# Performance work log

Measured on AMD Instinct MI355X. Metric: run time of the kernel, lower is better.

The kernel has to match this reference:

```python
import jax, jax.numpy as jnp
import numpy as np

THRESH = 8000.0  # saturating partial-sum accumulator threshold (thresh=8000 in source)
GROUP = 128      # channel chunk size used by split_tensor_* helpers
EPS = 1e-5

def binarize(x):
    # sign() forward with straight-through estimator (standard BinarizeConv2d behavior)
    return x + jax.lax.stop_gradient(jnp.sign(x) - x)

def psum_conv3x3(x, w):
    """3x3 'same' conv computed as 9 shifted-window partial sums per 128-channel
    group, with the running accumulator saturated to [-THRESH, THRESH] after each
    partial sum (emulating a low-bit hardware accumulator).
    x: [B, C, H, W]; w: [O, C, 3, 3] -> out [B, O, H, W]."""
    B, C, H, W = x.shape
    O = w.shape[0]
    xp = jnp.pad(x, ((0, 0), (0, 0), (1, 1), (1, 1)))
    acc = jnp.zeros((B, O, H, W), dtype=x.dtype)
    n_groups = C // GROUP
    for g in range(n_groups):
        xg = xp[:, g * GROUP:(g + 1) * GROUP]
        wg = w[:, g * GROUP:(g + 1) * GROUP]
        # split_tensor ordering: x1..x9 vary row (dim2) fastest, then col (dim3)
        for col in range(3):
            for row in range(3):
                part = jnp.einsum('bchw,oc->bohw',
                                  xg[:, :, row:row + H, col:col + W],
                                  wg[:, :, row, col])
                acc = jnp.clip(acc + part, -THRESH, THRESH)
    return acc

def batchnorm(x, gamma, beta, mean, var):
    inv = gamma / jnp.sqrt(var + EPS)
    return x * inv[None, :, None, None] + (beta - mean * inv)[None, :, None, None]

def setup_inputs() -> dict:
    key = jax.random.key(0)
    ks = jax.random.split(key, 12)
    B, C, H, W = 64, 128, 56, 56
    return {
        'x': jax.random.normal(ks[0], (B, C, H, W), jnp.float32),
        'w1': jax.random.normal(ks[1], (C, C, 3, 3), jnp.float32),
        'w2': jax.random.normal(ks[2], (C, C, 3, 3), jnp.float32),
        'gamma1': jax.random.uniform(ks[3], (C,), jnp.float32, 0.5, 1.5),
        'beta1': jax.random.normal(ks[4], (C,), jnp.float32) * 0.1,
        'mean1': jax.random.normal(ks[5], (C,), jnp.float32),
        'var1': jax.random.uniform(ks[6], (C,), jnp.float32, 0.5, 1.5),
        'gamma2': jax.random.uniform(ks[7], (C,), jnp.float32, 0.5, 1.5),
        'beta2': jax.random.normal(ks[8], (C,), jnp.float32) * 0.1,
        'mean2': jax.random.normal(ks[9], (C,), jnp.float32),
        'var2': jax.random.uniform(ks[10], (C,), jnp.float32, 0.5, 1.5),
    }

def reference(x, w1, w2, gamma1, beta1, mean1, var1, gamma2, beta2, mean2, var2):
    residual = x
    out = psum_conv3x3(binarize(x), binarize(w1))
    out = batchnorm(out, gamma1, beta1, mean1, var1)
    out = jnp.clip(out, -1.0, 1.0)  # hardtanh
    out = psum_conv3x3(binarize(out), binarize(w2))
    out = batchnorm(out, gamma2, beta2, mean2, var2)
    out = out + residual
    out = jnp.clip(out, -1.0, 1.0)
    return out
```

## Files before the change

kernel.cpp:

```cpp
#include <hip/hip_runtime.h>
#include <cstdint>
#include <cstddef>


typedef int      v4i __attribute__((ext_vector_type(4)));
typedef float    v4f __attribute__((ext_vector_type(4)));
typedef unsigned int v2u __attribute__((ext_vector_type(2)));

constexpr int B = 64, C = 128, H = 56, W = 56;
constexpr int HP = H + 2, WP = W + 2;
constexpr int PIX = H * W;
constexpr int M = B * H * W;
constexpr int NTILES = M / 256;
constexpr int TPX = NTILES / 8;

constexpr size_t XS_BYTES = (size_t)B * HP * WP * C;
constexpr size_t XS1_OFF = 0;
constexpr size_t XS2_OFF = XS_BYTES;
constexpr size_t WF_BYTES = 18 * 8192;
constexpr size_t WF1_OFF = 2 * XS_BYTES;
constexpr size_t WF2_OFF = WF1_OFF + WF_BYTES;
constexpr size_t BNP_OFF = WF2_OFF + WF_BYTES;

__global__ __launch_bounds__(256) void zero_halo(int8_t* __restrict__ xs1,
                                                 int8_t* __restrict__ xs2) {
    int b = blockIdx.x >> 2;
    int q = blockIdx.x & 3;
    int t = q * 256 + threadIdx.x;
    size_t ib = (size_t)b * HP * WP * C;
#pragma unroll
    for (int a = 0; a < 2; ++a) {
        uint32_t* p = (uint32_t*)((a ? xs2 : xs1) + ib);
        const int ROWD = WP * C / 4;
        for (int i = t; i < ROWD; i += 1024) {
            p[i] = 0;
            p[(HP - 1) * ROWD + i] = 0;
        }
        for (int i = t; i < 56 * 2 * 32; i += 1024) {
            int r = i >> 6;
            int side = (i >> 5) & 1;
            int j = i & 31;
            p[((r + 1) * WP + side * (WP - 1)) * (C / 4) + j] = 0;
        }
    }
}

__global__ __launch_bounds__(256) void prep_x(const float* __restrict__ x,
                                              int8_t* __restrict__ xs) {
    __shared__ uint32_t tl[256 * 33];
    int t = threadIdx.x;
    int m = blockIdx.x * 256 + t;
    int b_ = m / PIX, hw = m % PIX;
    const float* xp = x + (size_t)b_ * C * PIX + hw;
#pragma unroll
    for (int c4 = 0; c4 < 32; ++c4) {
        uint32_t v = 0;
#pragma unroll
        for (int j = 0; j < 4; ++j) {
            float f = __builtin_nontemporal_load(xp + (size_t)(c4 * 4 + j) * PIX);
            v |= ((uint32_t)(uint8_t)(int8_t)((f > 0.f) - (f < 0.f))) << (8 * j);
        }
        tl[t * 33 + c4] = v;
    }
    __syncthreads();
    int pl = t >> 3, co = t & 7;
#pragma unroll
    for (int pass = 0; pass < 8; ++pass) {
        int p = pass * 32 + pl;
        int mg = blockIdx.x * 256 + p;
        int b2 = mg / PIX, hw2 = mg % PIX, h2 = hw2 / W, w2 = hw2 % W;
        size_t ob = ((size_t)(b2 * HP + h2 + 1) * WP + (w2 + 1)) * C + co * 16;
        v4i val;
#pragma unroll
        for (int k = 0; k < 4; ++k) val[k] = (int)tl[p * 33 + co * 4 + k];
        *(v4i*)(xs + ob) = val;
    }
}

__global__ __launch_bounds__(256) void prep_w(
    const float* __restrict__ w1, const float* __restrict__ w2,
    const float* __restrict__ g1, const float* __restrict__ be1,
    const float* __restrict__ mu1, const float* __restrict__ va1,
    const float* __restrict__ g2, const float* __restrict__ be2,
    const float* __restrict__ mu2, const float* __restrict__ va2,
    int8_t* __restrict__ wf1, int8_t* __restrict__ wf2,
    float* __restrict__ bnp) {
    int t = blockIdx.x * 256 + threadIdx.x;
    if (t < 256) {
        int o = t & 127;
        if (t < 128) {
            float inv = g1[o] / sqrtf(va1[o] + 1e-5f);
            bnp[o]       = inv;
            bnp[128 + o] = __fsub_rn(be1[o], __fmul_rn(mu1[o], inv));
        } else {
            float inv = g2[o] / sqrtf(va2[o] + 1e-5f);
            bnp[256 + o] = inv;
            bnp[384 + o] = __fsub_rn(be2[o], __fmul_rn(mu2[o], inv));
        }
    }
    if (t >= 2 * 18 * 8 * 64) return;
    int lane = t & 63;
    int nsub = (t >> 6) & 7;
    int kh   = (t >> 9) & 1;
    int tap  = (t >> 10) % 9;
    int which = (t >> 10) / 9;
    const float* w = which ? w2 : w1;
    int8_t* wf = which ? wf2 : wf1;
    int o = (lane & 15) * 8 + nsub;
    int cbase = kh * 64 + (lane >> 4) * 16;
    int r = tap / 3, s = tap % 3;
    int slot = r * 6 + kh * 3 + s;
    int8_t frag[16];
#pragma unroll
    for (int j = 0; j < 16; ++j) {
        float f = w[((size_t)(o * C + cbase + j) * 3 + r) * 3 + s];
        frag[j] = (int8_t)((f > 0.f) - (f < 0.f));
    }
    *(v4i*)(wf + (size_t)((slot * 8 + nsub) * 64 + lane) * 16) =
        *(const v4i*)frag;
}

template <int PHASE, int RG>
__device__ __forceinline__ void do_tile(
    int mwave, const int8_t* __restrict__ xs, const int8_t* wlds,
    const float* binv, const float* btt, int lane, int quad, int l15,
    const float* __restrict__ xres, int8_t* __restrict__ xs_next,
    float* __restrict__ out)
{
    int abase[RG];
#pragma unroll
    for (int rg = 0; rg < RG; ++rg) {
        int ma = mwave + rg * 16 + l15;
        int wa = ma % W; int ta = ma / W; int ha = ta % H; int ba = ta / H;
        abase[rg] = ((ba * HP + ha) * WP + wa) * C + quad * 16;
    }
    int lidx = lane << 4;

    v4i acc[RG][8];
#pragma unroll
    for (int rg = 0; rg < RG; ++rg)
#pragma unroll
        for (int n = 0; n < 8; ++n) acc[rg][n] = (v4i)0;

    v4i a0[RG], a1[RG], bf0[8], bf1[8];
#pragma unroll
    for (int rg = 0; rg < RG; ++rg) a0[rg] = *(const v4i*)(xs + abase[rg]);
#pragma unroll
    for (int n = 0; n < 8; ++n)
        bf0[n] = *(const v4i*)(wlds + n * 1024 + lidx);
    __builtin_amdgcn_sched_barrier(0);

    const int8_t* wl = wlds;
    int aoffr = 0;
#pragma unroll 1
    for (int r3 = 0; r3 < 3; ++r3) {
#pragma unroll
        for (int kk = 0; kk < 6; ++kk) {
            const bool last = (r3 == 2) && (kk == 5);
            if (!last) {
                const int nkh = (kk + 1 < 6) ? ((kk + 1) / 3) : 0;
                const int ns  = (kk + 1 < 6) ? ((kk + 1) % 3) : 0;
                const int rbump = (kk + 1 < 6) ? 0 : WP * C;
                int naoff = aoffr + rbump + nkh * 64 + ns * C;
                const int8_t* lb = wl + (kk + 1) * 8192;
                if (((kk + 1) & 1) == 0) {
#pragma unroll
                    for (int rg = 0; rg < RG; ++rg)
                        a0[rg] = *(const v4i*)(xs + abase[rg] + naoff);
#pragma unroll
                    for (int n = 0; n < 8; ++n)
                        bf0[n] = *(const v4i*)(lb + n * 1024 + lidx);
                } else {
#pragma unroll
                    for (int rg = 0; rg < RG; ++rg)
                        a1[rg] = *(const v4i*)(xs + abase[rg] + naoff);
#pragma unroll
                    for (int n = 0; n < 8; ++n)
                        bf1[n] = *(const v4i*)(lb + n * 1024 + lidx);
                }
            }
            __builtin_amdgcn_sched_barrier(0);
            __builtin_amdgcn_s_setprio(1);
            if ((kk & 1) == 0) {
#pragma unroll
                for (int n = 0; n < 8; ++n)
#pragma unroll
                    for (int rg = 0; rg < RG; ++rg)
                        acc[rg][n] = __builtin_amdgcn_mfma_i32_16x16x64_i8(
                            a0[rg], bf0[n], acc[rg][n], 0, 0, 0);
            } else {
#pragma unroll
                for (int n = 0; n < 8; ++n)
#pragma unroll
                    for (int rg = 0; rg < RG; ++rg)
                        acc[rg][n] = __builtin_amdgcn_mfma_i32_16x16x64_i8(
                            a1[rg], bf1[n], acc[rg][n], 0, 0, 0);
            }
            __builtin_amdgcn_s_setprio(0);
            __builtin_amdgcn_sched_barrier(0);
        }
        aoffr += WP * C;
        wl += 6 * 8192;
    }

#pragma unroll
    for (int rg = 0; rg < RG; ++rg) {
        int m0 = mwave + rg * 16 + quad * 4;
        int w0 = m0 % W; int t0 = m0 / W; int h0 = t0 % H; int b0 = t0 / H;
        if (PHASE == 1) {
            int base = ((b0 * HP + h0 + 1) * WP + (w0 + 1)) * C + l15 * 8;
#pragma unroll
            for (int i = 0; i < 4; ++i) {
                uint32_t lo = 0, hi = 0;
#pragma unroll
                for (int n = 0; n < 8; ++n) {
                    float y = __fadd_rn(__fmul_rn((float)acc[rg][n][i], binv[n]), btt[n]);
                    uint32_t sb = (uint8_t)(int8_t)((y > 0.f) - (y < 0.f));
                    if (n < 4) lo |= sb << (8 * n);
                    else       hi |= sb << (8 * (n - 4));
                }
                v2u pk; pk[0] = lo; pk[1] = hi;
                *(v2u*)(xs_next + base + i * C) = pk;
            }
        } else {
            int pixb = b0 * C * PIX + h0 * W + w0;
#pragma unroll
            for (int n = 0; n < 8; ++n) {
                int idx = pixb + (l15 * 8 + n) * PIX;
                v4f r = __builtin_nontemporal_load((const v4f*)(xres + idx));
                v4f z;
#pragma unroll
                for (int i = 0; i < 4; ++i) {
                    float y = __fadd_rn(__fmul_rn((float)acc[rg][n][i], binv[n]), btt[n]);
                    float v = __fadd_rn(y, r[i]);
                    z[i] = fminf(fmaxf(v, -1.f), 1.f);
                }
                __builtin_nontemporal_store(z, (v4f*)(out + idx));
            }
        }
    }
}

template <int PHASE>
__global__ __launch_bounds__(512, 1) void conv_bin(
    const int8_t* __restrict__ xs,
    const int8_t* __restrict__ wf,
    const float* __restrict__ bnp,
    const float* __restrict__ xres,
    int8_t* __restrict__ xs_next,
    float* __restrict__ out)
{
    __shared__ int8_t wlds[18 * 8192];
    int t = threadIdx.x, lane = t & 63, wv = t >> 6;
    int quad = lane >> 4, l15 = lane & 15;

    {
        const v4i* g = (const v4i*)wf;
        v4i* l = (v4i*)wlds;
        for (int i = t; i < 18 * 512; i += 512) l[i] = g[i];
    }
    float binv[8], btt[8];
    {
        int o0 = (PHASE == 1 ? 0 : 256) + l15 * 8;
        int o1 = (PHASE == 1 ? 128 : 384) + l15 * 8;
#pragma unroll
        for (int n = 0; n < 8; ++n) { binv[n] = bnp[o0 + n]; btt[n] = bnp[o1 + n]; }
    }
    __syncthreads();

    int xcd = blockIdx.x & 7, local = blockIdx.x >> 3;
#pragma unroll 1
    for (int tloc = local; tloc < 96; tloc += 32) {
        int tile = xcd * TPX + tloc;
        do_tile<PHASE, 2>(tile * 256 + wv * 32, xs, wlds, binv, btt,
                          lane, quad, l15, xres, xs_next, out);
    }
    if (local < 4) {
        int tile = xcd * TPX + 96 + (local >> 1);
        int mw = tile * 256 + (local & 1) * 128 + wv * 16;
        do_tile<PHASE, 1>(mw, xs, wlds, binv, btt,
                          lane, quad, l15, xres, xs_next, out);
    }
}

extern "C" void kernel_launch(void* const* d_in, const int* in_sizes, int n_in,
                              void* d_out, int out_size, void* d_ws, size_t ws_size,
                              hipStream_t stream) {
    const float* x   = (const float*)d_in[0];
    const float* w1  = (const float*)d_in[1];
    const float* w2  = (const float*)d_in[2];
    const float* g1  = (const float*)d_in[3];
    const float* be1 = (const float*)d_in[4];
    const float* mu1 = (const float*)d_in[5];
    const float* va1 = (const float*)d_in[6];
    const float* g2  = (const float*)d_in[7];
    const float* be2 = (const float*)d_in[8];
    const float* mu2 = (const float*)d_in[9];
    const float* va2 = (const float*)d_in[10];

    int8_t* ws  = (int8_t*)d_ws;
    int8_t* xs1 = ws + XS1_OFF;
    int8_t* xs2 = ws + XS2_OFF;
    int8_t* wf1 = ws + WF1_OFF;
    int8_t* wf2 = ws + WF2_OFF;
    float*  bnp = (float*)(ws + BNP_OFF);

    zero_halo<<<256, 256, 0, stream>>>(xs1, xs2);
    prep_x<<<M / 256, 256, 0, stream>>>(x, xs1);
    prep_w<<<(2 * 18 * 8 * 64 + 255) / 256, 256, 0, stream>>>(
        w1, w2, g1, be1, mu1, va1, g2, be2, mu2, va2, wf1, wf2, bnp);

    conv_bin<1><<<256, 512, 0, stream>>>(xs1, wf1, bnp, nullptr, xs2, nullptr);
    conv_bin<2><<<256, 512, 0, stream>>>(xs2, wf2, bnp, x, nullptr, (float*)d_out);
}
```

Measured before the change: 322.7 us.

## Merge prep kernels into one launch and fold tail rows into last conv tile

Combines the halo zeroing, input binarize/transposition, and weight/BN preparation into a single prep kernel, cutting two kernel launches and their inter-kernel gaps. The conv kernel's tail work is also restructured: instead of a separate fourth pass with one row group for a few blocks, the leftover 16-row groups are folded into the third tile as a third row group, which shortens the critical path of the slowest blocks. The trade-off is that the third-tile variant holds more accumulators, raising register pressure, and the prep kernel now does strided halo writes from every thread.

```diff
diff --git a/kernel.cpp b/kernel.cpp
--- a/kernel.cpp
+++ b/kernel.cpp
@@ -22,73 +22,53 @@
 constexpr size_t WF2_OFF = WF1_OFF + WF_BYTES;
 constexpr size_t BNP_OFF = WF2_OFF + WF_BYTES;
 
-__global__ __launch_bounds__(256) void zero_halo(int8_t* __restrict__ xs1,
-                                                 int8_t* __restrict__ xs2) {
-    int b = blockIdx.x >> 2;
-    int q = blockIdx.x & 3;
-    int t = q * 256 + threadIdx.x;
-    size_t ib = (size_t)b * HP * WP * C;
-#pragma unroll
-    for (int a = 0; a < 2; ++a) {
-        uint32_t* p = (uint32_t*)((a ? xs2 : xs1) + ib);
-        const int ROWD = WP * C / 4;
-        for (int i = t; i < ROWD; i += 1024) {
-            p[i] = 0;
-            p[(HP - 1) * ROWD + i] = 0;
-        }
-        for (int i = t; i < 56 * 2 * 32; i += 1024) {
-            int r = i >> 6;
-            int side = (i >> 5) & 1;
-            int j = i & 31;
-            p[((r + 1) * WP + side * (WP - 1)) * (C / 4) + j] = 0;
-        }
-    }
-}
-
-__global__ __launch_bounds__(256) void prep_x(const float* __restrict__ x,
-                                              int8_t* __restrict__ xs) {
-    __shared__ uint32_t tl[256 * 33];
-    int t = threadIdx.x;
-    int m = blockIdx.x * 256 + t;
-    int b_ = m / PIX, hw = m % PIX;
-    const float* xp = x + (size_t)b_ * C * PIX + hw;
-#pragma unroll
-    for (int c4 = 0; c4 < 32; ++c4) {
-        uint32_t v = 0;
-#pragma unroll
-        for (int j = 0; j < 4; ++j) {
-            float f = __builtin_nontemporal_load(xp + (size_t)(c4 * 4 + j) * PIX);
-            v |= ((uint32_t)(uint8_t)(int8_t)((f > 0.f) - (f < 0.f))) << (8 * j);
-        }
-        tl[t * 33 + c4] = v;
-    }
-    __syncthreads();
-    int pl = t >> 3, co = t & 7;
-#pragma unroll
-    for (int pass = 0; pass < 8; ++pass) {
-        int p = pass * 32 + pl;
-        int mg = blockIdx.x * 256 + p;
-        int b2 = mg / PIX, hw2 = mg % PIX, h2 = hw2 / W, w2 = hw2 % W;
-        size_t ob = ((size_t)(b2 * HP + h2 + 1) * WP + (w2 + 1)) * C + co * 16;
-        v4i val;
-#pragma unroll
-        for (int k = 0; k < 4; ++k) val[k] = (int)tl[p * 33 + co * 4 + k];
-        *(v4i*)(xs + ob) = val;
-    }
-}
-
-__global__ __launch_bounds__(256) void prep_w(
+__global__ __launch_bounds__(256) void prep_all(
+    const float* __restrict__ x,
     const float* __restrict__ w1, const float* __restrict__ w2,
     const float* __restrict__ g1, const float* __restrict__ be1,
     const float* __restrict__ mu1, const float* __restrict__ va1,
     const float* __restrict__ g2, const float* __restrict__ be2,
     const float* __restrict__ mu2, const float* __restrict__ va2,
+    int8_t* __restrict__ xs1, int8_t* __restrict__ xs2,
     int8_t* __restrict__ wf1, int8_t* __restrict__ wf2,
-    float* __restrict__ bnp) {
-    int t = blockIdx.x * 256 + threadIdx.x;
-    if (t < 256) {
-        int o = t & 127;
-        if (t < 128) {
+    float* __restrict__ bnp)
+{
+    __shared__ uint32_t tl[256 * 33];
+    int t = threadIdx.x;
+    int tg = blockIdx.x * 256 + t;
+
+    {
+        int m = tg;
+        int b_ = m / PIX, hw = m % PIX;
+        const float* xp = x + (size_t)b_ * C * PIX + hw;
+#pragma unroll
+        for (int c4 = 0; c4 < 32; ++c4) {
+            uint32_t v = 0;
+#pragma unroll
+            for (int j = 0; j < 4; ++j) {
+                float f = __builtin_nontemporal_load(xp + (size_t)(c4 * 4 + j) * PIX);
+                v |= ((uint32_t)(uint8_t)(int8_t)((f > 0.f) - (f < 0.f))) << (8 * j);
+            }
+            tl[t * 33 + c4] = v;
+        }
+        __syncthreads();
+        int pl = t >> 3, co = t & 7;
+#pragma unroll
+        for (int pass = 0; pass < 8; ++pass) {
+            int p = pass * 32 + pl;
+            int mg = blockIdx.x * 256 + p;
+            int b2 = mg / PIX, hw2 = mg % PIX, h2 = hw2 / W, w2 = hw2 % W;
+            size_t ob = ((size_t)(b2 * HP + h2 + 1) * WP + (w2 + 1)) * C + co * 16;
+            v4i val;
+#pragma unroll
+            for (int k = 0; k < 4; ++k) val[k] = (int)tl[p * 33 + co * 4 + k];
+            *(v4i*)(xs1 + ob) = val;
+        }
+    }
+
+    if (tg < 256) {
+        int o = tg & 127;
+        if (tg < 128) {
             float inv = g1[o] / sqrtf(va1[o] + 1e-5f);
             bnp[o]       = inv;
             bnp[128 + o] = __fsub_rn(be1[o], __fmul_rn(mu1[o], inv));
@@ -98,31 +78,56 @@
             bnp[384 + o] = __fsub_rn(be2[o], __fmul_rn(mu2[o], inv));
         }
     }
-    if (t >= 2 * 18 * 8 * 64) return;
-    int lane = t & 63;
-    int nsub = (t >> 6) & 7;
-    int kh   = (t >> 9) & 1;
-    int tap  = (t >> 10) % 9;
-    int which = (t >> 10) / 9;
-    const float* w = which ? w2 : w1;
-    int8_t* wf = which ? wf2 : wf1;
-    int o = (lane & 15) * 8 + nsub;
-    int cbase = kh * 64 + (lane >> 4) * 16;
-    int r = tap / 3, s = tap % 3;
-    int slot = r * 6 + kh * 3 + s;
-    int8_t frag[16];
-#pragma unroll
-    for (int j = 0; j < 16; ++j) {
-        float f = w[((size_t)(o * C + cbase + j) * 3 + r) * 3 + s];
-        frag[j] = (int8_t)((f > 0.f) - (f < 0.f));
-    }
-    *(v4i*)(wf + (size_t)((slot * 8 + nsub) * 64 + lane) * 16) =
-        *(const v4i*)frag;
+
+    if (tg < 2 * 18 * 8 * 64) {
+        int lane = tg & 63;
+        int nsub = (tg >> 6) & 7;
+        int kh   = (tg >> 9) & 1;
+        int tap  = (tg >> 10) % 9;
+        int which = (tg >> 10) / 9;
+        const float* w = which ? w2 : w1;
+        int8_t* wf = which ? wf2 : wf1;
+        int o = (lane & 15) * 8 + nsub;
+        int cbase = kh * 64 + (lane >> 4) * 16;
+        int r = tap / 3, s = tap % 3;
+        int slot = r * 6 + kh * 3 + s;
+        int8_t frag[16];
+#pragma unroll
+        for (int j = 0; j < 16; ++j) {
+            float f = w[((size_t)(o * C + cbase + j) * 3 + r) * 3 + s];
+            frag[j] = (int8_t)((f > 0.f) - (f < 0.f));
+        }
+        *(v4i*)(wf + (size_t)((slot * 8 + nsub) * 64 + lane) * 16) =
+            *(const v4i*)frag;
+    }
+
+    {
+        constexpr int ROWD = WP * C / 4;
+        constexpr int HPI  = 2 * ROWD + 56 * 2 * 32;
+        constexpr int PERA = B * HPI;
+        constexpr int TOT  = 2 * PERA;
+        for (int i = tg; i < TOT; i += M) {
+            int a   = i / PERA;
+            int rem = i - a * PERA;
+            int b_  = rem / HPI;
+            int s   = rem - b_ * HPI;
+            uint32_t* p = (uint32_t*)((a ? xs2 : xs1) + (size_t)b_ * HP * WP * C);
+            if (s < ROWD) {
+                p[s] = 0;
+            } else if (s < 2 * ROWD) {
+                p[(HP - 1) * ROWD + (s - ROWD)] = 0;
+            } else {
+                int j = s - 2 * ROWD;
+                int r = j >> 6, side = (j >> 5) & 1, k = j & 31;
+                p[((r + 1) * WP + side * (WP - 1)) * (C / 4) + k] = 0;
+            }
+        }
+    }
 }
 
 template <int PHASE, int RG>
 __device__ __forceinline__ void do_tile(
-    int mwave, const int8_t* __restrict__ xs, const int8_t* wlds,
+    const int (&mrows)[RG], const int8_t* __restrict__ xs, const int8_t* wlds,
     const float* binv, const float* btt, int lane, int quad, int l15,
     const float* __restrict__ xres, int8_t* __restrict__ xs_next,
     float* __restrict__ out)
@@ -130,7 +135,7 @@
     int abase[RG];
 #pragma unroll
     for (int rg = 0; rg < RG; ++rg) {
-        int ma = mwave + rg * 16 + l15;
+        int ma = mrows[rg] + l15;
         int wa = ma % W; int ta = ma / W; int ha = ta % H; int ba = ta / H;
         abase[rg] = ((ba * HP + ha) * WP + wa) * C + quad * 16;
     }
@@ -205,7 +210,7 @@
 
 #pragma unroll
     for (int rg = 0; rg < RG; ++rg) {
-        int m0 = mwave + rg * 16 + quad * 4;
+        int m0 = mrows[rg] + quad * 4;
         int w0 = m0 % W; int t0 = m0 / W; int h0 = t0 % H; int b0 = t0 / H;
         if (PHASE == 1) {
             int base = ((b0 * HP + h0 + 1) * WP + (w0 + 1)) * C + l15 * 8;
@@ -269,17 +274,28 @@
     __syncthreads();
 
     int xcd = blockIdx.x & 7, local = blockIdx.x >> 3;
+
 #pragma unroll 1
-    for (int tloc = local; tloc < 96; tloc += 32) {
-        int tile = xcd * TPX + tloc;
-        do_tile<PHASE, 2>(tile * 256 + wv * 32, xs, wlds, binv, btt,
+    for (int rd = 0; rd < 2; ++rd) {
+        int tile = xcd * TPX + local + rd * 32;
+        int mw = tile * 256 + wv * 32;
+        int mrows2[2] = { mw, mw + 16 };
+        do_tile<PHASE, 2>(mrows2, xs, wlds, binv, btt,
                           lane, quad, l15, xres, xs_next, out);
     }
-    if (local < 4) {
-        int tile = xcd * TPX + 96 + (local >> 1);
-        int mw = tile * 256 + (local & 1) * 128 + wv * 16;
-        do_tile<PHASE, 1>(mw, xs, wlds, binv, btt,
-                          lane, quad, l15, xres, xs_next, out);
+    {
+        int tile = xcd * TPX + local + 64;
+        int mw = tile * 256 + wv * 32;
+        if (local < 4) {
+            int tailrow = (xcd * TPX + 96) * 256 + (local * 8 + wv) * 16;
+            int mrows3[3] = { mw, mw + 16, tailrow };
+            do_tile<PHASE, 3>(mrows3, xs, wlds, binv, btt,
+                              lane, quad, l15, xres, xs_next, out);
+        } else {
+            int mrows2[2] = { mw, mw + 16 };
+            do_tile<PHASE, 2>(mrows2, xs, wlds, binv, btt,
+                              lane, quad, l15, xres, xs_next, out);
+        }
     }
 }
 
@@ -305,10 +321,9 @@
     int8_t* wf2 = ws + WF2_OFF;
     float*  bnp = (float*)(ws + BNP_OFF);
 
-    zero_halo<<<256, 256, 0, stream>>>(xs1, xs2);
-    prep_x<<<M / 256, 256, 0, stream>>>(x, xs1);
-    prep_w<<<(2 * 18 * 8 * 64 + 255) / 256, 256, 0, stream>>>(
-        w1, w2, g1, be1, mu1, va1, g2, be2, mu2, va2, wf1, wf2, bnp);
+    prep_all<<<M / 256, 256, 0, stream>>>(
+        x, w1, w2, g1, be1, mu1, va1, g2, be2, mu2, va2,
+        xs1, xs2, wf1, wf2, bnp);
 
     conv_bin<1><<<256, 512, 0, stream>>>(xs1, wf1, bnp, nullptr, xs2, nullptr);
     conv_bin<2><<<256, 512, 0, stream>>>(xs2, wf2, bnp, x, nullptr, (float*)d_out);
```

Result: slower. 329.6 us (+2.2%).
